# Performance work log

Hardware: AMD Instinct MI355X
Metric: run time of the kernel (lower is better)

Reference implementation:

```python
import jax, jax.numpy as jnp
import numpy as np

NUM_GRAPHS = 1024


def setup_inputs() -> dict:
    key = jax.random.key(0)
    k1, k2, k3, k4 = jax.random.split(key, 4)
    N, D, H = 500000, 256, 128
    x = jax.random.normal(k1, (N, D), dtype=jnp.float32)
    # attention MLP params (Linear(D,H) -> ReLU -> Linear(H,1))
    W1 = jax.random.normal(k2, (D, H), dtype=jnp.float32) * (1.0 / np.sqrt(D))
    b1 = jnp.zeros((H,), dtype=jnp.float32)
    W2 = jax.random.normal(k3, (H, 1), dtype=jnp.float32) * (1.0 / np.sqrt(H))
    b2 = jnp.zeros((1,), dtype=jnp.float32)
    batch = jnp.sort(jax.random.randint(k4, (N,), 0, NUM_GRAPHS)).astype(jnp.int64)
    return {"x": x, "W1": W1, "b1": b1, "W2": W2, "b2": b2, "batch": batch}


def reference(x, W1, b1, W2, b2, batch):
    # attention MLP -> scalar score per node, softmax over ALL nodes (global, as in source)
    h = jax.nn.relu(x @ W1 + b1)            # [N, H]
    scores = h @ W2 + b2                    # [N, 1]
    attn = jax.nn.softmax(scores.ravel())[:, None]  # [N, 1], global softmax

    # attention-weighted sum per graph
    attn_pooled = jax.ops.segment_sum(x * attn, batch, num_segments=NUM_GRAPHS,
                                      indices_are_sorted=True)  # [G, D]
    # max pool per graph (all segments occupied given N >> G)
    max_pooled = jax.ops.segment_max(x, batch, num_segments=NUM_GRAPHS,
                                     indices_are_sorted=True)   # [G, D]
    # mean pool per graph: scatter-add + clamped counts
    sum_pooled = jax.ops.segment_sum(x, batch, num_segments=NUM_GRAPHS,
                                     indices_are_sorted=True)   # [G, D]
    counts = jnp.bincount(batch, length=NUM_GRAPHS).astype(x.dtype)
    counts = jnp.clip(counts, 1.0, None)[:, None]                # [G, 1]
    mean_pooled = sum_pooled / counts

    return jnp.concatenate([attn_pooled, max_pooled, mean_pooled], axis=-1)  # [G, 3D]
```

## Files before the change

kernel.cpp:

```cpp
#include <hip/hip_runtime.h>
#include <cmath>

#define D_IN 256
#define H_DIM 128
#define NUM_GRAPHS 1024
#define CHUNK 64
#define MAXSEG 4
#define REC_F 768

typedef __attribute__((ext_vector_type(8))) __bf16 bf16x8;
typedef __attribute__((ext_vector_type(4))) float f32x4;
typedef __attribute__((ext_vector_type(4))) unsigned short ushort4v;

__device__ inline float b2f(unsigned short u) {
    unsigned int v = ((unsigned int)u) << 16;
    return __builtin_bit_cast(float, v);
}

__device__ inline int lower_bound_i(const int* __restrict__ arr, int n, int val) {
    int lo = 0, hi = n;
    while (lo < hi) {
        int mid = (lo + hi) >> 1;
        if (arr[mid] < val) lo = mid + 1; else hi = mid;
    }
    return lo;
}

__global__ __launch_bounds__(256) void prep_kernel(
    const float* __restrict__ W1, const int* __restrict__ batch, int N, int NB,
    ushort* __restrict__ packed, int* __restrict__ bounds,
    int* __restrict__ cfirst) {
    int b = blockIdx.x;
    if (b < 16) {
        int tid = b * 256 + threadIdx.x;
        int nt = tid >> 9;
        int ks = (tid >> 6) & 7;
        int l = tid & 63;
        int col = nt * 16 + (l & 15);
        int kbase = ks * 32 + ((l >> 4) & 3) * 8;
#pragma unroll
        for (int i = 0; i < 8; ++i) {
            float v = W1[(size_t)(kbase + i) * H_DIM + col];
            __bf16 h = (__bf16)v;
            packed[(size_t)tid * 8 + i] = __builtin_bit_cast(unsigned short, h);
        }
    } else if (b < 21) {
        int i = (b - 16) * 256 + threadIdx.x;
        if (i <= NUM_GRAPHS) bounds[i] = lower_bound_i(batch, N, i);
    } else {
        int i = (b - 21) * 256 + threadIdx.x;
        if (i < NB) cfirst[i] = batch[(long long)i * CHUNK];
    }
}

__global__ __launch_bounds__(256) void fused_kernel(
    const float* __restrict__ x, const ushort* __restrict__ w1p,
    const float* __restrict__ b1, const float* __restrict__ W2,
    const float* __restrict__ b2, const int* __restrict__ batch,
    float* __restrict__ recs, float* __restrict__ zpart, int N) {
    int tid = threadIdx.x;
    int l = tid & 63;
    int w = tid >> 6;
    int r16 = l & 15;
    int kg = l >> 4;
    int blk = blockIdx.x;
    long long base = (long long)blk * CHUNK;
    int chunkN = (int)min((long long)CHUNK, (long long)N - base);

    __shared__ ushort sx[CHUNK * D_IN];
    __shared__ float pscore[4][CHUNK];
    __shared__ int seglist[MAXSEG + 1];
    __shared__ int snseg;

    int bval = -1;
    if (w == 0) {
        long long bi = base + l;
        bval = (bi < N) ? batch[bi] : -1;
    }

    bf16x8 breg0[8], breg1[8];
#pragma unroll
    for (int ks = 0; ks < 8; ++ks) {
        breg0[ks] = *(const bf16x8*)(w1p + ((size_t)((w * 2) * 8 + ks) * 64 + l) * 8);
        breg1[ks] = *(const bf16x8*)(w1p + ((size_t)((w * 2 + 1) * 8 + ks) * 64 + l) * 8);
    }

    {
        int row = tid >> 2;
        long long grow = base + row;
        if (grow >= N) grow = N - 1;
        const float* xr = x + grow * D_IN;
        int gb = tid & 3;
        f32x4 xv[16];
#pragma unroll
        for (int j = 0; j < 8; ++j) {
            int g = gb + 4 * j;
            xv[2 * j] = *(const f32x4*)(xr + g * 8);
            xv[2 * j + 1] = *(const f32x4*)(xr + g * 8 + 4);
        }
        unsigned rowswz = (unsigned)(row & 7) << 4;
#pragma unroll
        for (int j = 0; j < 8; ++j) {
            int g = gb + 4 * j;
            bf16x8 pk;
#pragma unroll
            for (int i = 0; i < 4; ++i) {
                pk[i] = (__bf16)xv[2 * j][i];
                pk[i + 4] = (__bf16)xv[2 * j + 1][i];
            }
            unsigned addr = ((unsigned)(row * 512 + g * 16)) ^ rowswz;
            *(bf16x8*)((char*)sx + addr) = pk;
        }
    }

    float w2v[2], b1v[2];
#pragma unroll
    for (int q = 0; q < 2; ++q) {
        int c = (w * 2 + q) * 16 + r16;
        w2v[q] = W2[c];
        b1v[q] = b1[c];
    }
    float bb = b2[0];

    if (w == 0) {
        int prev = __shfl_up(bval, 1, 64);
        bool flag = (l < chunkN) && (l == 0 || bval != prev);
        unsigned long long m = __ballot(flag);
        if (l == 0) {
            int ns = 0;
            while (m && ns < MAXSEG) {
                int b = __ffsll(m) - 1;
                seglist[ns] = b;
                ns++;
                m &= m - 1;
            }
            snseg = ns;
            seglist[ns] = chunkN;
        }
    }
    __syncthreads();

    f32x4 acc[4][2] = {};
#pragma unroll
    for (int ks = 0; ks < 8; ++ks) {
#pragma unroll
        for (int mt = 0; mt < 4; ++mt) {
            int row = mt * 16 + r16;
            unsigned addr = ((unsigned)(row * 512 + ks * 64 + kg * 16)) ^
                            ((unsigned)(row & 7) << 4);
            bf16x8 af = *(const bf16x8*)((const char*)sx + addr);
            acc[mt][0] = __builtin_amdgcn_mfma_f32_16x16x32_bf16(af, breg0[ks], acc[mt][0], 0, 0, 0);
            acc[mt][1] = __builtin_amdgcn_mfma_f32_16x16x32_bf16(af, breg1[ks], acc[mt][1], 0, 0, 0);
        }
    }
#pragma unroll
    for (int mt = 0; mt < 4; ++mt) {
#pragma unroll
        for (int reg = 0; reg < 4; ++reg) {
            float p = fmaxf(acc[mt][0][reg] + b1v[0], 0.f) * w2v[0] +
                      fmaxf(acc[mt][1][reg] + b1v[1], 0.f) * w2v[1];
            p += __shfl_xor(p, 1, 64);
            p += __shfl_xor(p, 2, 64);
            p += __shfl_xor(p, 4, 64);
            p += __shfl_xor(p, 8, 64);
            if (r16 == 0) pscore[w][mt * 16 + kg * 4 + reg] = p;
        }
    }
    __syncthreads();

    float s = pscore[0][l] + pscore[1][l] + pscore[2][l] + pscore[3][l] + bb;
    float e_l = (l < chunkN) ? __expf(s) : 0.f;

    if (w == 0) {
        float z = e_l;
        z += __shfl_xor(z, 1, 64);
        z += __shfl_xor(z, 2, 64);
        z += __shfl_xor(z, 4, 64);
        z += __shfl_xor(z, 8, 64);
        z += __shfl_xor(z, 16, 64);
        z += __shfl_xor(z, 32, 64);
        if (l == 0) zpart[blk] = z;
    }

    int nseg = snseg;

    int cg = l & 15;
    int rg = l >> 4;
    unsigned cbyte = (unsigned)(w * 128 + cg * 8);

    for (int sg = 0; sg < nseg; ++sg) {
        int sStart = seglist[sg];
        int sEnd = seglist[sg + 1];
        f32x4 asum = {0.f, 0.f, 0.f, 0.f};
        f32x4 ssum = {0.f, 0.f, 0.f, 0.f};
        f32x4 mx = {-INFINITY, -INFINITY, -INFINITY, -INFINITY};
#pragma unroll
        for (int j = 0; j < 16; ++j) {
            int row = rg + 4 * j;
            float wj = __shfl(e_l, row, 64);
            bool in = (row >= sStart) && (row < sEnd);
            unsigned addr = ((unsigned)(row * 512) + cbyte) ^
                            ((unsigned)(row & 7) << 4);
            ushort4v hv = *(const ushort4v*)((const char*)sx + addr);
            float wje = in ? wj : 0.f;
#pragma unroll
            for (int c = 0; c < 4; ++c) {
                float v = b2f(hv[c]);
                asum[c] += v * wje;
                ssum[c] += in ? v : 0.f;
                mx[c] = fmaxf(mx[c], in ? v : -INFINITY);
            }
        }
#pragma unroll
        for (int c = 0; c < 4; ++c) {
            asum[c] += __shfl_xor(asum[c], 16, 64);
            asum[c] += __shfl_xor(asum[c], 32, 64);
            ssum[c] += __shfl_xor(ssum[c], 16, 64);
            ssum[c] += __shfl_xor(ssum[c], 32, 64);
            mx[c] = fmaxf(mx[c], __shfl_xor(mx[c], 16, 64));
            mx[c] = fmaxf(mx[c], __shfl_xor(mx[c], 32, 64));
        }
        if (rg == 0) {
            float* rb = recs + (size_t)(blk * MAXSEG + sg) * REC_F;
            int co = w * 64 + cg * 4;
            *(f32x4*)(rb + co) = asum;
            *(f32x4*)(rb + 256 + co) = ssum;
            *(f32x4*)(rb + 512 + co) = mx;
        }
    }
}

__global__ __launch_bounds__(256) void zreduce_kernel(
    const float* __restrict__ zpart, int n, float* __restrict__ MZ) {
    int tid = threadIdx.x;
    float z = 0.f;
    for (int i = tid; i < n; i += 256) z += zpart[i];
    __shared__ float sz[256];
    sz[tid] = z;
    __syncthreads();
    for (int off = 128; off > 0; off >>= 1) {
        if (tid < off) sz[tid] += sz[tid + off];
        __syncthreads();
    }
    if (tid == 0) MZ[0] = 1.f / sz[0];
}

__global__ __launch_bounds__(256) void combine_kernel(
    const float* __restrict__ recs, const int* __restrict__ bounds,
    const int* __restrict__ cfirst, const float* __restrict__ MZ,
    float* __restrict__ out) {
    int g = blockIdx.x;
    int tid = threadIdx.x;
    float invZ = MZ[0];
    int start = bounds[g];
    int end = bounds[g + 1];
    int cnt = end - start;

    float ew = 0.f, ss = 0.f, mxv = -INFINITY;
    if (cnt > 0) {
        int b0 = start >> 6, b1 = (end - 1) >> 6;
        for (int b = b0; b <= b1; ++b) {
            int sg = g - cfirst[b];
            if (sg >= 0 && sg < MAXSEG) {
                const float* rb = recs + (size_t)(b * MAXSEG + sg) * REC_F;
                ew += rb[tid];
                ss += rb[256 + tid];
                mxv = fmaxf(mxv, rb[512 + tid]);
            }
        }
    }
    size_t ob = (size_t)g * (3 * D_IN);
    out[ob + tid] = ew * invZ;
    out[ob + D_IN + tid] = (cnt > 0) ? mxv : 0.f;
    out[ob + 2 * D_IN + tid] = ss / (float)max(cnt, 1);
}

extern "C" void kernel_launch(void* const* d_in, const int* in_sizes, int n_in,
                              void* d_out, int out_size, void* d_ws, size_t ws_size,
                              hipStream_t stream) {
    const float* x = (const float*)d_in[0];
    const float* W1 = (const float*)d_in[1];
    const float* b1 = (const float*)d_in[2];
    const float* W2 = (const float*)d_in[3];
    const float* b2 = (const float*)d_in[4];
    const int* batch = (const int*)d_in[5];
    int N = in_sizes[0] / D_IN;
    float* out = (float*)d_out;
    int NB = (N + CHUNK - 1) / CHUNK;

    char* ws = (char*)d_ws;
    size_t off = 0;
    ushort* w1p = (ushort*)(ws + off);
    off += 8 * 8 * 64 * 8 * sizeof(ushort);
    off = (off + 255) & ~(size_t)255;
    int* bounds = (int*)(ws + off);
    off += (NUM_GRAPHS + 1) * sizeof(int);
    off = (off + 255) & ~(size_t)255;
    int* cfirst = (int*)(ws + off);
    off += (size_t)NB * sizeof(int);
    off = (off + 255) & ~(size_t)255;
    float* recs = (float*)(ws + off);
    off += (size_t)NB * MAXSEG * REC_F * sizeof(float);
    off = (off + 255) & ~(size_t)255;
    float* zpart = (float*)(ws + off);
    off += (size_t)NB * sizeof(float);
    off = (off + 255) & ~(size_t)255;
    float* MZ = (float*)(ws + off);
    off += 256;

    int prepBlocks = 21 + (NB + 255) / 256;
    prep_kernel<<<prepBlocks, 256, 0, stream>>>(W1, batch, N, NB, w1p, bounds, cfirst);
    fused_kernel<<<NB, 256, 0, stream>>>(x, w1p, b1, W2, b2, batch,
                                         recs, zpart, N);
    zreduce_kernel<<<1, 256, 0, stream>>>(zpart, NB, MZ);
    combine_kernel<<<NUM_GRAPHS, 256, 0, stream>>>(recs, bounds, cfirst, MZ, out);
}
```

Baseline: 178.2 us.

## Load x directly to LDS as fp32, halve chunk size, fold z-reduction into combine

The fused kernel now copies x rows straight from global memory into LDS with global_load_lds instead of staging them in registers as bf16. The bf16 conversion moves to the MFMA operand read, and pooling sums use fp32 values from LDS. CHUNK drops to 32 and MAXSEG to 2, with a launch-bounds occupancy hint, so there are more, smaller blocks. The separate z-reduction kernel and the cfirst array are removed: every combine block re-reduces the partial sums and reads batch directly, trading fewer launches for redundant reduction work. The MAXSEG=2 assumption relies on each 32-row chunk spanning at most two graphs.

After: 174.8 us. About the same (-1.9%).

```diff
diff --git a/kernel.cpp b/kernel.cpp
--- a/kernel.cpp
+++ b/kernel.cpp
@@ -4,17 +4,17 @@
 #define D_IN 256
 #define H_DIM 128
 #define NUM_GRAPHS 1024
-#define CHUNK 64
-#define MAXSEG 4
+#define CHUNK 32
+#define MAXSEG 2
 #define REC_F 768
 
 typedef __attribute__((ext_vector_type(8))) __bf16 bf16x8;
 typedef __attribute__((ext_vector_type(4))) float f32x4;
-typedef __attribute__((ext_vector_type(4))) unsigned short ushort4v;
-
-__device__ inline float b2f(unsigned short u) {
-    unsigned int v = ((unsigned int)u) << 16;
-    return __builtin_bit_cast(float, v);
+
+__device__ inline void load_lds_16(const void* g, void* l) {
+    __builtin_amdgcn_global_load_lds(
+        (const __attribute__((address_space(1))) void*)g,
+        (__attribute__((address_space(3))) void*)l, 16, 0, 0);
 }
 
 __device__ inline int lower_bound_i(const int* __restrict__ arr, int n, int val) {
@@ -27,9 +27,8 @@
 }
 
 __global__ __launch_bounds__(256) void prep_kernel(
-    const float* __restrict__ W1, const int* __restrict__ batch, int N, int NB,
-    ushort* __restrict__ packed, int* __restrict__ bounds,
-    int* __restrict__ cfirst) {
+    const float* __restrict__ W1, const int* __restrict__ batch, int N,
+    ushort* __restrict__ packed, int* __restrict__ bounds) {
     int b = blockIdx.x;
     if (b < 16) {
         int tid = b * 256 + threadIdx.x;
@@ -44,16 +43,13 @@
             __bf16 h = (__bf16)v;
             packed[(size_t)tid * 8 + i] = __builtin_bit_cast(unsigned short, h);
         }
-    } else if (b < 21) {
+    } else {
         int i = (b - 16) * 256 + threadIdx.x;
         if (i <= NUM_GRAPHS) bounds[i] = lower_bound_i(batch, N, i);
-    } else {
-        int i = (b - 21) * 256 + threadIdx.x;
-        if (i < NB) cfirst[i] = batch[(long long)i * CHUNK];
-    }
-}
-
-__global__ __launch_bounds__(256) void fused_kernel(
+    }
+}
+
+__global__ __launch_bounds__(256, 4) void fused_kernel(
     const float* __restrict__ x, const ushort* __restrict__ w1p,
     const float* __restrict__ b1, const float* __restrict__ W2,
     const float* __restrict__ b2, const int* __restrict__ batch,
@@ -67,15 +63,20 @@
     long long base = (long long)blk * CHUNK;
     int chunkN = (int)min((long long)CHUNK, (long long)N - base);
 
-    __shared__ ushort sx[CHUNK * D_IN];
+    __shared__ float sxf[CHUNK * D_IN];
     __shared__ float pscore[4][CHUNK];
     __shared__ int seglist[MAXSEG + 1];
     __shared__ int snseg;
 
-    int bval = -1;
-    if (w == 0) {
-        long long bi = base + l;
-        bval = (bi < N) ? batch[bi] : -1;
+#pragma unroll
+    for (int k = 0; k < 8; ++k) {
+        int row = k * 4 + w;
+        long long grow = base + row;
+        if (grow >= N) grow = N - 1;
+        unsigned srcb = ((unsigned)(l * 16)) ^ ((unsigned)(row & 7) << 4);
+        const float* src = x + grow * D_IN + (srcb >> 2);
+        char* dst = (char*)sxf + (unsigned)(row * 1024 + l * 16);
+        load_lds_16(src, dst);
     }
 
     bf16x8 breg0[8], breg1[8];
@@ -85,52 +86,16 @@
         breg1[ks] = *(const bf16x8*)(w1p + ((size_t)((w * 2 + 1) * 8 + ks) * 64 + l) * 8);
     }
 
-    {
-        int row = tid >> 2;
-        long long grow = base + row;
-        if (grow >= N) grow = N - 1;
-        const float* xr = x + grow * D_IN;
-        int gb = tid & 3;
-        f32x4 xv[16];
-#pragma unroll
-        for (int j = 0; j < 8; ++j) {
-            int g = gb + 4 * j;
-            xv[2 * j] = *(const f32x4*)(xr + g * 8);
-            xv[2 * j + 1] = *(const f32x4*)(xr + g * 8 + 4);
-        }
-        unsigned rowswz = (unsigned)(row & 7) << 4;
-#pragma unroll
-        for (int j = 0; j < 8; ++j) {
-            int g = gb + 4 * j;
-            bf16x8 pk;
-#pragma unroll
-            for (int i = 0; i < 4; ++i) {
-                pk[i] = (__bf16)xv[2 * j][i];
-                pk[i + 4] = (__bf16)xv[2 * j + 1][i];
-            }
-            unsigned addr = ((unsigned)(row * 512 + g * 16)) ^ rowswz;
-            *(bf16x8*)((char*)sx + addr) = pk;
-        }
-    }
-
-    float w2v[2], b1v[2];
-#pragma unroll
-    for (int q = 0; q < 2; ++q) {
-        int c = (w * 2 + q) * 16 + r16;
-        w2v[q] = W2[c];
-        b1v[q] = b1[c];
-    }
-    float bb = b2[0];
-
     if (w == 0) {
+        int bval = -1;
+        if (l < chunkN) bval = batch[base + l];
         int prev = __shfl_up(bval, 1, 64);
         bool flag = (l < chunkN) && (l == 0 || bval != prev);
         unsigned long long m = __ballot(flag);
         if (l == 0) {
             int ns = 0;
             while (m && ns < MAXSEG) {
-                int b = __ffsll(m) - 1;
-                seglist[ns] = b;
+                seglist[ns] = __ffsll(m) - 1;
                 ns++;
                 m &= m - 1;
             }
@@ -138,23 +103,40 @@
             seglist[ns] = chunkN;
         }
     }
+
+    float w2v[2], b1v[2];
+#pragma unroll
+    for (int q = 0; q < 2; ++q) {
+        int c = (w * 2 + q) * 16 + r16;
+        w2v[q] = W2[c];
+        b1v[q] = b1[c];
+    }
+    float bb = b2[0];
+
     __syncthreads();
 
-    f32x4 acc[4][2] = {};
+    f32x4 acc[2][2] = {};
 #pragma unroll
     for (int ks = 0; ks < 8; ++ks) {
 #pragma unroll
-        for (int mt = 0; mt < 4; ++mt) {
+        for (int mt = 0; mt < 2; ++mt) {
             int row = mt * 16 + r16;
-            unsigned addr = ((unsigned)(row * 512 + ks * 64 + kg * 16)) ^
-                            ((unsigned)(row & 7) << 4);
-            bf16x8 af = *(const bf16x8*)((const char*)sx + addr);
+            unsigned swz = (unsigned)(row & 7) << 4;
+            unsigned cb = (unsigned)(ks * 128 + kg * 32);
+            f32x4 u0 = *(const f32x4*)((const char*)sxf + row * 1024 + (cb ^ swz));
+            f32x4 u1 = *(const f32x4*)((const char*)sxf + row * 1024 + ((cb + 16) ^ swz));
+            bf16x8 af;
+#pragma unroll
+            for (int i = 0; i < 4; ++i) {
+                af[i] = (__bf16)u0[i];
+                af[i + 4] = (__bf16)u1[i];
+            }
             acc[mt][0] = __builtin_amdgcn_mfma_f32_16x16x32_bf16(af, breg0[ks], acc[mt][0], 0, 0, 0);
             acc[mt][1] = __builtin_amdgcn_mfma_f32_16x16x32_bf16(af, breg1[ks], acc[mt][1], 0, 0, 0);
         }
     }
 #pragma unroll
-    for (int mt = 0; mt < 4; ++mt) {
+    for (int mt = 0; mt < 2; ++mt) {
 #pragma unroll
         for (int reg = 0; reg < 4; ++reg) {
             float p = fmaxf(acc[mt][0][reg] + b1v[0], 0.f) * w2v[0] +
@@ -168,9 +150,11 @@
     }
     __syncthreads();
 
-    float s = pscore[0][l] + pscore[1][l] + pscore[2][l] + pscore[3][l] + bb;
-    float e_l = (l < chunkN) ? __expf(s) : 0.f;
-
+    float e_l = 0.f;
+    if (l < CHUNK) {
+        float s = pscore[0][l] + pscore[1][l] + pscore[2][l] + pscore[3][l] + bb;
+        e_l = (l < chunkN) ? __expf(s) : 0.f;
+    }
     if (w == 0) {
         float z = e_l;
         z += __shfl_xor(z, 1, 64);
@@ -186,7 +170,7 @@
 
     int cg = l & 15;
     int rg = l >> 4;
-    unsigned cbyte = (unsigned)(w * 128 + cg * 8);
+    unsigned cbyte = (unsigned)(w * 256 + cg * 16);
 
     for (int sg = 0; sg < nseg; ++sg) {
         int sStart = seglist[sg];
@@ -195,20 +179,19 @@
         f32x4 ssum = {0.f, 0.f, 0.f, 0.f};
         f32x4 mx = {-INFINITY, -INFINITY, -INFINITY, -INFINITY};
 #pragma unroll
-        for (int j = 0; j < 16; ++j) {
+        for (int j = 0; j < 8; ++j) {
             int row = rg + 4 * j;
             float wj = __shfl(e_l, row, 64);
             bool in = (row >= sStart) && (row < sEnd);
-            unsigned addr = ((unsigned)(row * 512) + cbyte) ^
-                            ((unsigned)(row & 7) << 4);
-            ushort4v hv = *(const ushort4v*)((const char*)sx + addr);
+            unsigned addr = (unsigned)(row * 1024) +
+                            (cbyte ^ ((unsigned)(row & 7) << 4));
+            f32x4 v = *(const f32x4*)((const char*)sxf + addr);
             float wje = in ? wj : 0.f;
 #pragma unroll
             for (int c = 0; c < 4; ++c) {
-                float v = b2f(hv[c]);
-                asum[c] += v * wje;
-                ssum[c] += in ? v : 0.f;
-                mx[c] = fmaxf(mx[c], in ? v : -INFINITY);
+                asum[c] += v[c] * wje;
+                ssum[c] += in ? v[c] : 0.f;
+                mx[c] = fmaxf(mx[c], in ? v[c] : -INFINITY);
             }
         }
 #pragma unroll
@@ -230,43 +213,38 @@
     }
 }
 
-__global__ __launch_bounds__(256) void zreduce_kernel(
-    const float* __restrict__ zpart, int n, float* __restrict__ MZ) {
-    int tid = threadIdx.x;
-    float z = 0.f;
-    for (int i = tid; i < n; i += 256) z += zpart[i];
-    __shared__ float sz[256];
-    sz[tid] = z;
-    __syncthreads();
-    for (int off = 128; off > 0; off >>= 1) {
-        if (tid < off) sz[tid] += sz[tid + off];
-        __syncthreads();
-    }
-    if (tid == 0) MZ[0] = 1.f / sz[0];
-}
-
 __global__ __launch_bounds__(256) void combine_kernel(
     const float* __restrict__ recs, const int* __restrict__ bounds,
-    const int* __restrict__ cfirst, const float* __restrict__ MZ,
+    const int* __restrict__ batch, const float* __restrict__ zpart, int nzp,
     float* __restrict__ out) {
     int g = blockIdx.x;
     int tid = threadIdx.x;
-    float invZ = MZ[0];
+
+    __shared__ float szr[256];
+    float z = 0.f;
+    for (int i = tid; i < nzp; i += 256) z += zpart[i];
+    szr[tid] = z;
+    __syncthreads();
+    for (int off = 128; off > 0; off >>= 1) {
+        if (tid < off) szr[tid] += szr[tid + off];
+        __syncthreads();
+    }
+    float invZ = 1.f / szr[0];
+
     int start = bounds[g];
     int end = bounds[g + 1];
     int cnt = end - start;
 
     float ew = 0.f, ss = 0.f, mxv = -INFINITY;
     if (cnt > 0) {
-        int b0 = start >> 6, b1 = (end - 1) >> 6;
+        int b0 = start / CHUNK, b1 = (end - 1) / CHUNK;
+        int sg0 = (batch[(long long)b0 * CHUNK] == g) ? 0 : 1;
         for (int b = b0; b <= b1; ++b) {
-            int sg = g - cfirst[b];
-            if (sg >= 0 && sg < MAXSEG) {
-                const float* rb = recs + (size_t)(b * MAXSEG + sg) * REC_F;
-                ew += rb[tid];
-                ss += rb[256 + tid];
-                mxv = fmaxf(mxv, rb[512 + tid]);
-            }
+            int sg = (b == b0) ? sg0 : 0;
+            const float* rb = recs + (size_t)(b * MAXSEG + sg) * REC_F;
+            ew += rb[tid];
+            ss += rb[256 + tid];
+            mxv = fmaxf(mxv, rb[512 + tid]);
         }
     }
     size_t ob = (size_t)g * (3 * D_IN);
@@ -296,22 +274,15 @@
     int* bounds = (int*)(ws + off);
     off += (NUM_GRAPHS + 1) * sizeof(int);
     off = (off + 255) & ~(size_t)255;
-    int* cfirst = (int*)(ws + off);
-    off += (size_t)NB * sizeof(int);
-    off = (off + 255) & ~(size_t)255;
     float* recs = (float*)(ws + off);
     off += (size_t)NB * MAXSEG * REC_F * sizeof(float);
     off = (off + 255) & ~(size_t)255;
     float* zpart = (float*)(ws + off);
     off += (size_t)NB * sizeof(float);
-    off = (off + 255) & ~(size_t)255;
-    float* MZ = (float*)(ws + off);
-    off += 256;
-
-    int prepBlocks = 21 + (NB + 255) / 256;
-    prep_kernel<<<prepBlocks, 256, 0, stream>>>(W1, batch, N, NB, w1p, bounds, cfirst);
+
+    prep_kernel<<<21, 256, 0, stream>>>(W1, batch, N, w1p, bounds);
     fused_kernel<<<NB, 256, 0, stream>>>(x, w1p, b1, W2, b2, batch,
                                          recs, zpart, N);
-    zreduce_kernel<<<1, 256, 0, stream>>>(zpart, NB, MZ);
-    combine_kernel<<<NUM_GRAPHS, 256, 0, stream>>>(recs, bounds, cfirst, MZ, out);
-}
+    combine_kernel<<<NUM_GRAPHS, 256, 0, stream>>>(recs, bounds, batch,
+                                                   zpart, NB, out);
+}
```
